# Kernel optimization log

Measured on AMD Instinct MI355X. Metric: run time of the kernel, lower is better.

## Reference

```python
import jax, jax.numpy as jnp
import numpy as np

N = 100000          # nodes
E = 625000          # edges
D_IN = 128
D_H = 128
D_OUT = 10
NUM_GRAPHS = 256


def setup_inputs() -> dict:
    key = jax.random.key(0)
    ks = jax.random.split(key, 12)
    x = jax.random.normal(ks[0], (N, D_IN), dtype=jnp.float32)
    edge_index = jax.random.randint(ks[1], (2, E), 0, N, dtype=jnp.int32)
    batch = jnp.sort(jax.random.randint(ks[2], (N,), 0, NUM_GRAPHS, dtype=jnp.int32))
    s_in = 1.0 / np.sqrt(D_IN)
    s_h = 1.0 / np.sqrt(D_H)
    # nn.Linear weights are [out, in]; kept that layout, applied as x @ W.T
    W1_0 = jax.random.uniform(ks[3], (D_H, D_IN), jnp.float32, -s_in, s_in)
    W2_0 = jax.random.uniform(ks[4], (D_H, D_IN), jnp.float32, -s_in, s_in)
    W1_1 = jax.random.uniform(ks[5], (D_H, D_H), jnp.float32, -s_h, s_h)
    W2_1 = jax.random.uniform(ks[6], (D_H, D_H), jnp.float32, -s_h, s_h)
    W1_2 = jax.random.uniform(ks[7], (D_H, D_H), jnp.float32, -s_h, s_h)
    W2_2 = jax.random.uniform(ks[8], (D_H, D_H), jnp.float32, -s_h, s_h)
    Wc = jax.random.uniform(ks[9], (D_OUT, D_H), jnp.float32, -s_h, s_h)
    bc = jax.random.uniform(ks[10], (D_OUT,), jnp.float32, -s_h, s_h)
    return {"x": x, "edge_index": edge_index, "batch": batch,
            "W1_0": W1_0, "W2_0": W2_0, "W1_1": W1_1, "W2_1": W2_1,
            "W1_2": W1_2, "W2_2": W2_2, "Wc": Wc, "bc": bc}


def _layer_f(x, row, col, W1, W2):
    # self term + sum-aggregated neighbor term, ReLU
    self_feat = x @ W1.T                       # [N, D]
    nbr_feat = (x @ W2.T)[col]                 # gather per edge: [E, D]
    agg = jax.ops.segment_sum(nbr_feat, row, num_segments=N)  # scatter-add
    return jax.nn.relu(self_feat + agg)


def reference(x, edge_index, batch, W1_0, W2_0, W1_1, W2_1, W1_2, W2_2, Wc, bc):
    row, col = edge_index[0], edge_index[1]
    h = _layer_f(x, row, col, W1_0, W2_0)
    h = _layer_f(h, row, col, W1_1, W2_1)
    h = _layer_f(h, row, col, W1_2, W2_2)
    # global mean pool per graph
    sums = jax.ops.segment_sum(h, batch, num_segments=NUM_GRAPHS)  # [G, D]
    counts = jax.ops.segment_sum(jnp.ones((N,), h.dtype), batch, num_segments=NUM_GRAPHS)
    pooled = sums / jnp.maximum(counts, 1.0)[:, None]
    return pooled @ Wc.T + bc                  # [G, D_OUT]
```

## Files before the change

kernel.cpp:

```cpp
#include <hip/hip_runtime.h>

#define NNODES 100000
#define NEDGES 625000
#define DFEAT  128
#define NGRAPH 256
#define DOUTC  10

typedef __attribute__((ext_vector_type(8))) short bf16x8;
typedef __attribute__((ext_vector_type(4))) float f32x4;
typedef __attribute__((ext_vector_type(8))) ushort ushort8v;

__device__ __forceinline__ ushort f2bf(float f) {
    __bf16 b = (__bf16)f;
    return __builtin_bit_cast(ushort, b);
}
__device__ __forceinline__ float bf2f(ushort u) {
    return __builtin_bit_cast(float, (uint)u << 16);
}

__global__ __launch_bounds__(256) void convert_all(const float* __restrict__ x,
                                                   const float* __restrict__ w0,
                                                   const float* __restrict__ w1,
                                                   const float* __restrict__ w2,
                                                   const float* __restrict__ w3,
                                                   const float* __restrict__ w4,
                                                   const float* __restrict__ w5,
                                                   ushort* __restrict__ Wb,
                                                   ushort* __restrict__ Hb,
                                                   float* __restrict__ gsum,
                                                   int* __restrict__ deg,
                                                   int* __restrict__ counter) {
    const int tid = blockIdx.x * 256 + threadIdx.x;
    const int NT = gridDim.x * 256;
    if (tid == 0) *counter = 0;
    const float* ptrs[6] = {w0, w1, w2, w3, w4, w5};
    for (int i = tid; i < 6 * DFEAT * DFEAT; i += NT) {
        int m = i >> 14, j = i & 16383;
        Wb[i] = f2bf(ptrs[m][j]);
    }
    for (int i = tid; i < NGRAPH * DFEAT; i += NT) gsum[i] = 0.f;
    for (int i = tid; i < NNODES; i += NT) deg[i] = 0;
    const int n8 = NNODES * DFEAT / 8;
    for (int i = tid; i < n8; i += NT) {
        float4 a = *(const float4*)&x[(size_t)i * 8];
        float4 b = *(const float4*)&x[(size_t)i * 8 + 4];
        ushort8v o;
        o[0] = f2bf(a.x); o[1] = f2bf(a.y); o[2] = f2bf(a.z); o[3] = f2bf(a.w);
        o[4] = f2bf(b.x); o[5] = f2bf(b.y); o[6] = f2bf(b.z); o[7] = f2bf(b.w);
        *(ushort8v*)&Hb[(size_t)i * 8] = o;
    }
}

__global__ __launch_bounds__(256) void histo_kernel(const int* __restrict__ rows,
                                                    int* __restrict__ deg) {
    int i = blockIdx.x * 256 + threadIdx.x;
    if (i < NEDGES) atomicAdd(&deg[rows[i]], 1);
}

__global__ __launch_bounds__(256) void alloc_ranges(const int* __restrict__ deg,
                                                    int* __restrict__ offs,
                                                    int* __restrict__ cursor,
                                                    int* __restrict__ counter) {
    __shared__ int red[256];
    __shared__ int baseSh;
    int t = threadIdx.x;
    int i = blockIdx.x * 256 + t;
    int v = (i < NNODES) ? deg[i] : 0;
    red[t] = v;
    __syncthreads();
    int x = v;
    for (int off = 1; off < 256; off <<= 1) {
        int y = (t >= off) ? red[t - off] : 0;
        __syncthreads();
        x += y;
        red[t] = x;
        __syncthreads();
    }
    if (t == 255) baseSh = atomicAdd(counter, x);
    __syncthreads();
    int pos = baseSh + x - v;
    if (i < NNODES) { offs[i] = pos; cursor[i] = pos; }
}

__global__ __launch_bounds__(256) void scatter_edges(const int* __restrict__ rows,
                                                     const int* __restrict__ cols,
                                                     int* __restrict__ cursor,
                                                     int* __restrict__ scol) {
    int i = blockIdx.x * 256 + threadIdx.x;
    if (i < NEDGES) {
        int p = atomicAdd(&cursor[rows[i]], 1);
        scol[p] = cols[i];
    }
}

__global__ __launch_bounds__(256) void aggregate_g16(const ushort* __restrict__ Hb,
                                                     const int* __restrict__ offs,
                                                     const int* __restrict__ deg,
                                                     const int* __restrict__ scol,
                                                     ushort* __restrict__ Ab) {
    int node = blockIdx.x * 16 + (threadIdx.x >> 4);
    int l = threadIdx.x & 15;
    if (node >= NNODES) return;
    int beg = offs[node];
    int end = beg + deg[node];
    float a[8] = {};
    int e = beg;
    for (; e + 4 <= end; e += 4) {
        int c0 = scol[e];
        int c1 = scol[e + 1];
        int c2 = scol[e + 2];
        int c3 = scol[e + 3];
        ushort8v v0 = *(const ushort8v*)&Hb[(size_t)c0 * DFEAT + l * 8];
        ushort8v v1 = *(const ushort8v*)&Hb[(size_t)c1 * DFEAT + l * 8];
        ushort8v v2 = *(const ushort8v*)&Hb[(size_t)c2 * DFEAT + l * 8];
        ushort8v v3 = *(const ushort8v*)&Hb[(size_t)c3 * DFEAT + l * 8];
#pragma unroll
        for (int j = 0; j < 8; ++j)
            a[j] += (bf2f(v0[j]) + bf2f(v1[j])) + (bf2f(v2[j]) + bf2f(v3[j]));
    }
    for (; e < end; ++e) {
        int c0 = scol[e];
        ushort8v v0 = *(const ushort8v*)&Hb[(size_t)c0 * DFEAT + l * 8];
#pragma unroll
        for (int j = 0; j < 8; ++j) a[j] += bf2f(v0[j]);
    }
    ushort8v o;
#pragma unroll
    for (int j = 0; j < 8; ++j) o[j] = f2bf(a[j]);
    *(ushort8v*)&Ab[(size_t)node * DFEAT + l * 8] = o;
}

__global__ __launch_bounds__(256, 3) void fused_dual_gemm_lds(const ushort* __restrict__ Hin,
                                                              const ushort* __restrict__ Ab,
                                                              const ushort* __restrict__ W1b,
                                                              const ushort* __restrict__ W2b,
                                                              ushort* __restrict__ Hout) {
    __shared__ char lds[8192];
    const int tid = threadIdx.x;
    const int wid = tid >> 6;
    const int lane = tid & 63;
    const int l15 = lane & 15, lhi = lane >> 4;

    bf16x8 w1[2][4], w2[2][4];
#pragma unroll
    for (int ot = 0; ot < 2; ++ot)
#pragma unroll
        for (int ks = 0; ks < 4; ++ks) {
            int orow = wid * 32 + (l15 >> 2) * 8 + ot * 4 + (l15 & 3);
            w1[ot][ks] = *(const bf16x8*)&W1b[orow * DFEAT + ks * 32 + lhi * 8];
            w2[ot][ks] = *(const bf16x8*)&W2b[orow * DFEAT + ks * 32 + lhi * 8];
        }
#pragma unroll
    for (int ot = 0; ot < 2; ++ot)
#pragma unroll
        for (int ks = 0; ks < 4; ++ks) {
            asm volatile("" : "+v"(w1[ot][ks]));
            asm volatile("" : "+v"(w2[ot][ks]));
        }

    const int sr = tid >> 4;
    const int sj = (tid & 15) * 16;
    const int swz = sj ^ ((sr & 7) << 4);
    int roff[4];
#pragma unroll
    for (int ks = 0; ks < 4; ++ks)
        roff[ks] = l15 * 256 + ((ks * 64 + lhi * 16) ^ ((l15 & 7) << 4));

    const int ntiles = NNODES / 16;
    for (int t = blockIdx.x; t < ntiles; t += gridDim.x) {
        size_t tileByte = (size_t)t * 16 * 256;
        ushort8v hv = *(const ushort8v*)((const char*)Hin + tileByte + sr * 256 + sj);
        ushort8v av = *(const ushort8v*)((const char*)Ab + tileByte + sr * 256 + sj);
        __syncthreads();
        *(ushort8v*)&lds[sr * 256 + swz] = hv;
        *(ushort8v*)&lds[4096 + sr * 256 + swz] = av;
        __syncthreads();

        bf16x8 hfr[4], afr[4];
#pragma unroll
        for (int ks = 0; ks < 4; ++ks) {
            hfr[ks] = *(const bf16x8*)&lds[roff[ks]];
            afr[ks] = *(const bf16x8*)&lds[4096 + roff[ks]];
        }
        f32x4 acc0 = {}, acc1 = {};
#pragma unroll
        for (int ks = 0; ks < 4; ++ks)
            acc0 = __builtin_amdgcn_mfma_f32_16x16x32_bf16(w1[0][ks], hfr[ks], acc0, 0, 0, 0);
#pragma unroll
        for (int ks = 0; ks < 4; ++ks)
            acc0 = __builtin_amdgcn_mfma_f32_16x16x32_bf16(w2[0][ks], afr[ks], acc0, 0, 0, 0);
#pragma unroll
        for (int ks = 0; ks < 4; ++ks)
            acc1 = __builtin_amdgcn_mfma_f32_16x16x32_bf16(w1[1][ks], hfr[ks], acc1, 0, 0, 0);
#pragma unroll
        for (int ks = 0; ks < 4; ++ks)
            acc1 = __builtin_amdgcn_mfma_f32_16x16x32_bf16(w2[1][ks], afr[ks], acc1, 0, 0, 0);
        ushort8v p;
        p[0] = f2bf(fmaxf(acc0.x, 0.f));
        p[1] = f2bf(fmaxf(acc0.y, 0.f));
        p[2] = f2bf(fmaxf(acc0.z, 0.f));
        p[3] = f2bf(fmaxf(acc0.w, 0.f));
        p[4] = f2bf(fmaxf(acc1.x, 0.f));
        p[5] = f2bf(fmaxf(acc1.y, 0.f));
        p[6] = f2bf(fmaxf(acc1.z, 0.f));
        p[7] = f2bf(fmaxf(acc1.w, 0.f));
        *(ushort8v*)&Hout[(size_t)(t * 16 + l15) * DFEAT + wid * 32 + lhi * 8] = p;
    }
}

__global__ __launch_bounds__(256) void pool_partial(const ushort* __restrict__ Hb,
                                                    const int* __restrict__ batch,
                                                    float* __restrict__ gsum) {
    int wave = (blockIdx.x * 256 + threadIdx.x) >> 6;
    int lane = threadIdx.x & 63;
    int base = wave * 64;
    if (base >= NNODES) return;
    int end = min(base + 64, NNODES);
    const uint* Hp = (const uint*)Hb + lane;
    float ax = 0.f, ay = 0.f;
    int gprev = batch[base];
    for (int n = base; n < end; ++n) {
        int g = batch[n];
        if (g != gprev) {
            atomicAdd(&gsum[gprev * DFEAT + lane * 2], ax);
            atomicAdd(&gsum[gprev * DFEAT + lane * 2 + 1], ay);
            ax = 0.f; ay = 0.f; gprev = g;
        }
        uint v = Hp[(size_t)n * 64];
        ax += __builtin_bit_cast(float, v << 16);
        ay += __builtin_bit_cast(float, v & 0xffff0000u);
    }
    atomicAdd(&gsum[gprev * DFEAT + lane * 2], ax);
    atomicAdd(&gsum[gprev * DFEAT + lane * 2 + 1], ay);
}

__global__ __launch_bounds__(128) void pool_classify2(const float* __restrict__ gsum,
                                                      const int* __restrict__ batch,
                                                      const float* __restrict__ Wc,
                                                      const float* __restrict__ bc,
                                                      float* __restrict__ out) {
    int g = blockIdx.x;
    int f = threadIdx.x;
    __shared__ int bounds[2];
    if (f < 2) {
        int target = g + f;
        int lo = 0, hi = NNODES;
        while (lo < hi) {
            int mid = (lo + hi) >> 1;
            if (batch[mid] < target) lo = mid + 1; else hi = mid;
        }
        bounds[f] = lo;
    }
    __syncthreads();
    float cnt = (float)(bounds[1] - bounds[0]);
    float pooled = gsum[g * DFEAT + f] / fmaxf(cnt, 1.0f);

    __shared__ float red[128];
    for (int o = 0; o < DOUTC; ++o) {
        red[f] = pooled * Wc[o * DFEAT + f];
        __syncthreads();
        for (int off = 64; off > 0; off >>= 1) {
            if (f < off) red[f] += red[f + off];
            __syncthreads();
        }
        if (f == 0) out[g * DOUTC + o] = red[0] + bc[o];
        __syncthreads();
    }
}

extern "C" void kernel_launch(void* const* d_in, const int* in_sizes, int n_in,
                              void* d_out, int out_size, void* d_ws, size_t ws_size,
                              hipStream_t stream) {
    const float* x    = (const float*)d_in[0];
    const int*   ei   = (const int*)d_in[1];
    const int*   batch= (const int*)d_in[2];
    const float* Wc   = (const float*)d_in[9];
    const float* bc   = (const float*)d_in[10];
    float* out = (float*)d_out;

    const int* rows = ei;
    const int* cols = ei + NEDGES;

    char* ws = (char*)d_ws;
    ushort* Hb = (ushort*)ws;  ws += (size_t)NNODES * DFEAT * sizeof(ushort);
    ushort* Hc = (ushort*)ws;  ws += (size_t)NNODES * DFEAT * sizeof(ushort);
    ushort* Ab = (ushort*)ws;  ws += (size_t)NNODES * DFEAT * sizeof(ushort);
    ushort* Wb = (ushort*)ws;  ws += (size_t)6 * DFEAT * DFEAT * sizeof(ushort);
    float* gsum = (float*)ws;  ws += (size_t)NGRAPH * DFEAT * sizeof(float);
    int* deg    = (int*)ws;    ws += (size_t)NNODES * sizeof(int);
    int* offs   = (int*)ws;    ws += (size_t)NNODES * sizeof(int);
    int* cursor = (int*)ws;    ws += (size_t)NNODES * sizeof(int);
    int* scol   = (int*)ws;    ws += (size_t)NEDGES * sizeof(int);
    int* counter= (int*)ws;    ws += 64;

    convert_all<<<784, 256, 0, stream>>>(x,
        (const float*)d_in[3], (const float*)d_in[4], (const float*)d_in[5],
        (const float*)d_in[6], (const float*)d_in[7], (const float*)d_in[8],
        Wb, Hb, gsum, deg, counter);

    histo_kernel<<<(NEDGES + 255) / 256, 256, 0, stream>>>(rows, deg);
    alloc_ranges<<<(NNODES + 255) / 256, 256, 0, stream>>>(deg, offs, cursor, counter);
    scatter_edges<<<(NEDGES + 255) / 256, 256, 0, stream>>>(rows, cols, cursor, scol);

    const int aggGrid  = (NNODES + 15) / 16;
    const int gemmGrid = 768;
    const ushort* hcur = Hb;
    ushort* hnext = Hc;
    for (int l = 0; l < 3; ++l) {
        const ushort* w1 = Wb + (size_t)(2 * l) * DFEAT * DFEAT;
        const ushort* w2 = Wb + (size_t)(2 * l + 1) * DFEAT * DFEAT;
        aggregate_g16<<<aggGrid, 256, 0, stream>>>(hcur, offs, deg, scol, Ab);
        fused_dual_gemm_lds<<<gemmGrid, 256, 0, stream>>>(hcur, Ab, w1, w2, hnext);
        const ushort* tmp = hcur; hcur = hnext; hnext = (ushort*)tmp;
    }

    const int poolWaves = (NNODES + 63) / 64;
    pool_partial<<<(poolWaves * 64 + 255) / 256, 256, 0, stream>>>(hcur, batch, gsum);
    pool_classify2<<<NGRAPH, 128, 0, stream>>>(gsum, batch, Wc, bc, out);
}
```

Before: 260.3 us.

## Fuse global mean-pool accumulation into the last layer's dual GEMM epilogue

The last layer's GEMM no longer writes its output to memory. Instead its epilogue does a segmented reduction of the ReLU'd bf16-rounded values per graph id, using shuffles within each 16-row tile, and atomically adds the partial sums into gsum. This removes the separate pool_partial kernel along with one store and one reload of the full hidden matrix. In exchange it adds a shuffle-reduction loop and atomics inside the GEMM, which may raise register pressure and lengthen that kernel.

```diff
diff --git a/kernel.cpp b/kernel.cpp
--- a/kernel.cpp
+++ b/kernel.cpp
@@ -208,30 +208,119 @@
     }
 }
 
-__global__ __launch_bounds__(256) void pool_partial(const ushort* __restrict__ Hb,
-                                                    const int* __restrict__ batch,
-                                                    float* __restrict__ gsum) {
-    int wave = (blockIdx.x * 256 + threadIdx.x) >> 6;
-    int lane = threadIdx.x & 63;
-    int base = wave * 64;
-    if (base >= NNODES) return;
-    int end = min(base + 64, NNODES);
-    const uint* Hp = (const uint*)Hb + lane;
-    float ax = 0.f, ay = 0.f;
-    int gprev = batch[base];
-    for (int n = base; n < end; ++n) {
-        int g = batch[n];
-        if (g != gprev) {
-            atomicAdd(&gsum[gprev * DFEAT + lane * 2], ax);
-            atomicAdd(&gsum[gprev * DFEAT + lane * 2 + 1], ay);
-            ax = 0.f; ay = 0.f; gprev = g;
-        }
-        uint v = Hp[(size_t)n * 64];
-        ax += __builtin_bit_cast(float, v << 16);
-        ay += __builtin_bit_cast(float, v & 0xffff0000u);
-    }
-    atomicAdd(&gsum[gprev * DFEAT + lane * 2], ax);
-    atomicAdd(&gsum[gprev * DFEAT + lane * 2 + 1], ay);
+__global__ __launch_bounds__(256, 3) void fused_dual_gemm_lds_pool(
+        const ushort* __restrict__ Hin,
+        const ushort* __restrict__ Ab,
+        const ushort* __restrict__ W1b,
+        const ushort* __restrict__ W2b,
+        const int* __restrict__ batch,
+        float* __restrict__ gsum) {
+    __shared__ char lds[8192];
+    const int tid = threadIdx.x;
+    const int wid = tid >> 6;
+    const int lane = tid & 63;
+    const int l15 = lane & 15, lhi = lane >> 4;
+    const int f0 = wid * 32 + lhi * 8;
+
+    bf16x8 w1[2][4], w2[2][4];
+#pragma unroll
+    for (int ot = 0; ot < 2; ++ot)
+#pragma unroll
+        for (int ks = 0; ks < 4; ++ks) {
+            int orow = wid * 32 + (l15 >> 2) * 8 + ot * 4 + (l15 & 3);
+            w1[ot][ks] = *(const bf16x8*)&W1b[orow * DFEAT + ks * 32 + lhi * 8];
+            w2[ot][ks] = *(const bf16x8*)&W2b[orow * DFEAT + ks * 32 + lhi * 8];
+        }
+#pragma unroll
+    for (int ot = 0; ot < 2; ++ot)
+#pragma unroll
+        for (int ks = 0; ks < 4; ++ks) {
+            asm volatile("" : "+v"(w1[ot][ks]));
+            asm volatile("" : "+v"(w2[ot][ks]));
+        }
+
+    const int sr = tid >> 4;
+    const int sj = (tid & 15) * 16;
+    const int swz = sj ^ ((sr & 7) << 4);
+    int roff[4];
+#pragma unroll
+    for (int ks = 0; ks < 4; ++ks)
+        roff[ks] = l15 * 256 + ((ks * 64 + lhi * 16) ^ ((l15 & 7) << 4));
+
+    const int ntiles = NNODES / 16;
+    for (int t = blockIdx.x; t < ntiles; t += gridDim.x) {
+        size_t tileByte = (size_t)t * 16 * 256;
+        ushort8v hv = *(const ushort8v*)((const char*)Hin + tileByte + sr * 256 + sj);
+        ushort8v av = *(const ushort8v*)((const char*)Ab + tileByte + sr * 256 + sj);
+        __syncthreads();
+        *(ushort8v*)&lds[sr * 256 + swz] = hv;
+        *(ushort8v*)&lds[4096 + sr * 256 + swz] = av;
+        __syncthreads();
+
+        bf16x8 hfr[4], afr[4];
+#pragma unroll
+        for (int ks = 0; ks < 4; ++ks) {
+            hfr[ks] = *(const bf16x8*)&lds[roff[ks]];
+            afr[ks] = *(const bf16x8*)&lds[4096 + roff[ks]];
+        }
+        f32x4 acc0 = {}, acc1 = {};
+#pragma unroll
+        for (int ks = 0; ks < 4; ++ks)
+            acc0 = __builtin_amdgcn_mfma_f32_16x16x32_bf16(w1[0][ks], hfr[ks], acc0, 0, 0, 0);
+#pragma unroll
+        for (int ks = 0; ks < 4; ++ks)
+            acc0 = __builtin_amdgcn_mfma_f32_16x16x32_bf16(w2[0][ks], afr[ks], acc0, 0, 0, 0);
+#pragma unroll
+        for (int ks = 0; ks < 4; ++ks)
+            acc1 = __builtin_amdgcn_mfma_f32_16x16x32_bf16(w1[1][ks], hfr[ks], acc1, 0, 0, 0);
+#pragma unroll
+        for (int ks = 0; ks < 4; ++ks)
+            acc1 = __builtin_amdgcn_mfma_f32_16x16x32_bf16(w2[1][ks], afr[ks], acc1, 0, 0, 0);
+
+        float v0 = bf2f(f2bf(fmaxf(acc0.x, 0.f)));
+        float v1 = bf2f(f2bf(fmaxf(acc0.y, 0.f)));
+        float v2 = bf2f(f2bf(fmaxf(acc0.z, 0.f)));
+        float v3 = bf2f(f2bf(fmaxf(acc0.w, 0.f)));
+        float v4 = bf2f(f2bf(fmaxf(acc1.x, 0.f)));
+        float v5 = bf2f(f2bf(fmaxf(acc1.y, 0.f)));
+        float v6 = bf2f(f2bf(fmaxf(acc1.z, 0.f)));
+        float v7 = bf2f(f2bf(fmaxf(acc1.w, 0.f)));
+
+        int g = batch[t * 16 + l15];
+        int remaining = 0xFFFF;
+        while (remaining) {
+            int lead = __ffs(remaining) - 1;
+            int gl = __shfl(g, (lane & 48) | lead, 64);
+            bool mine = (g == gl);
+            float s0 = mine ? v0 : 0.f, s1 = mine ? v1 : 0.f;
+            float s2 = mine ? v2 : 0.f, s3 = mine ? v3 : 0.f;
+            float s4 = mine ? v4 : 0.f, s5 = mine ? v5 : 0.f;
+            float s6 = mine ? v6 : 0.f, s7 = mine ? v7 : 0.f;
+#pragma unroll
+            for (int off = 1; off < 16; off <<= 1) {
+                s0 += __shfl_xor(s0, off, 64);
+                s1 += __shfl_xor(s1, off, 64);
+                s2 += __shfl_xor(s2, off, 64);
+                s3 += __shfl_xor(s3, off, 64);
+                s4 += __shfl_xor(s4, off, 64);
+                s5 += __shfl_xor(s5, off, 64);
+                s6 += __shfl_xor(s6, off, 64);
+                s7 += __shfl_xor(s7, off, 64);
+            }
+            if (l15 == lead) {
+                float* gp = &gsum[gl * DFEAT + f0];
+                atomicAdd(gp + 0, s0);
+                atomicAdd(gp + 1, s1);
+                atomicAdd(gp + 2, s2);
+                atomicAdd(gp + 3, s3);
+                atomicAdd(gp + 4, s4);
+                atomicAdd(gp + 5, s5);
+                atomicAdd(gp + 6, s6);
+                atomicAdd(gp + 7, s7);
+            }
+            remaining &= ~((int)(__ballot(mine) & 0xFFFFull));
+        }
+    }
 }
 
 __global__ __launch_bounds__(128) void pool_classify2(const float* __restrict__ gsum,
@@ -306,15 +395,19 @@
     const int gemmGrid = 768;
     const ushort* hcur = Hb;
     ushort* hnext = Hc;
-    for (int l = 0; l < 3; ++l) {
+    for (int l = 0; l < 2; ++l) {
         const ushort* w1 = Wb + (size_t)(2 * l) * DFEAT * DFEAT;
         const ushort* w2 = Wb + (size_t)(2 * l + 1) * DFEAT * DFEAT;
         aggregate_g16<<<aggGrid, 256, 0, stream>>>(hcur, offs, deg, scol, Ab);
         fused_dual_gemm_lds<<<gemmGrid, 256, 0, stream>>>(hcur, Ab, w1, w2, hnext);
         const ushort* tmp = hcur; hcur = hnext; hnext = (ushort*)tmp;
     }
-
-    const int poolWaves = (NNODES + 63) / 64;
-    pool_partial<<<(poolWaves * 64 + 255) / 256, 256, 0, stream>>>(hcur, batch, gsum);
+    {
+        const ushort* w1 = Wb + (size_t)4 * DFEAT * DFEAT;
+        const ushort* w2 = Wb + (size_t)5 * DFEAT * DFEAT;
+        aggregate_g16<<<aggGrid, 256, 0, stream>>>(hcur, offs, deg, scol, Ab);
+        fused_dual_gemm_lds_pool<<<gemmGrid, 256, 0, stream>>>(hcur, Ab, w1, w2, batch, gsum);
+    }
+
     pool_classify2<<<NGRAPH, 128, 0, stream>>>(gsum, batch, Wc, bc, out);
 }
```

Result: no change. 259.0 us (-0.5%).
